# Kernel optimization log

Measured on AMD Instinct MI355X. Metric: run time of the kernel, lower is better.

## Reference

```python
import jax, jax.numpy as jnp
import numpy as np

EPS = 1e-5

def _layernorm(x, g, b):
    mu = jnp.mean(x, axis=-1, keepdims=True)
    var = jnp.mean((x - mu) ** 2, axis=-1, keepdims=True)
    return (x - mu) * jax.lax.rsqrt(var + EPS) * g + b

def setup_inputs() -> dict:
    key = jax.random.key(0)
    ks = jax.random.split(key, 12)
    B, N, C, n = 2, 1024, 256, 100
    x = jax.random.normal(ks[0], (B, N, C), dtype=jnp.float32)
    query = jax.random.normal(ks[1], (n, B, C), dtype=jnp.float32)
    policy = jax.random.uniform(ks[2], (B, N, 1), dtype=jnp.float32)
    s = lambda k, shp: jax.random.normal(k, shp, dtype=jnp.float32) * (1.0 / np.sqrt(shp[0]))
    return {
        "x": x, "query": query, "policy": policy,
        "ln_g": jnp.ones((C,), jnp.float32), "ln_b": jnp.zeros((C,), jnp.float32),
        "W_in": s(ks[3], (C, C)), "b_in": jnp.zeros((C,), jnp.float32),
        "W1": s(ks[4], (2 * C, C)), "b1": jnp.zeros((C,), jnp.float32),
        "W2": s(ks[5], (C, C // 2)), "b2": jnp.zeros((C // 2,), jnp.float32),
        "W3": s(ks[6], (C // 2, 2)), "b3": jnp.zeros((2,), jnp.float32),
    }

def reference(x, query, policy, ln_g, ln_b, W_in, b_in, W1, b1, W2, b2, W3, b3):
    B, N, C = x.shape
    n = query.shape[0]
    q = jnp.transpose(query, (1, 0, 2))  # [B, n, C]
    # in_conv: LayerNorm -> Linear -> GELU. The torch code repeats x across the
    # query dim first, but the math is identical per query, so compute once.
    h = jax.nn.gelu(_layernorm(x, ln_g, ln_b) @ W_in + b_in, approximate=False)  # [B, N, C]
    half = C // 2
    local_x = h[:, :, :half]  # [B, N, C/2]
    # policy-weighted masked pooling (policy identical across queries)
    glob = jnp.sum(h[:, :, half:] * policy, axis=1, keepdims=True) / jnp.sum(policy, axis=1, keepdims=True)  # [B, 1, C/2]
    feature = jnp.concatenate([
        jnp.broadcast_to(local_x[:, None, :, :], (B, n, N, half)),
        jnp.broadcast_to(glob[:, None, :, :], (B, n, N, half)),
        jnp.broadcast_to(q[:, :, None, :], (B, n, N, C)),
    ], axis=-1)  # [B, n, N, 2C]
    z = jax.nn.gelu(feature @ W1 + b1, approximate=False)
    z = jax.nn.gelu(z @ W2 + b2, approximate=False)
    z = z @ W3 + b3
    return jax.nn.log_softmax(z, axis=-1)  # [B, n, N, 2]
```

## Files before the change

### kernel.cpp

```cpp
#include <hip/hip_runtime.h>
#include <math.h>

#define BB 2
#define NN 1024
#define CC 256
#define NQ 100
#define HALF 128

typedef __attribute__((ext_vector_type(8))) short bf16x8;
typedef __attribute__((ext_vector_type(4))) float f32x4;

__device__ __forceinline__ float exp2_fast(float v) {
#if __has_builtin(__builtin_amdgcn_exp2f)
    return __builtin_amdgcn_exp2f(v);
#else
    return __expf(0.69314718056f * v);
#endif
}

__device__ __forceinline__ float gelu_fast(float x) {
    float x2 = x * x;
    float v = x * fmaf(0.10293942f, x2, 2.30211418f);
    float e = exp2_fast(v);
    float r = __builtin_amdgcn_rcpf(1.0f + e);
    return fmaf(-x, r, x);
}

__device__ __forceinline__ short f2bf(float f) {
    union { float f; unsigned u; } v; v.f = f;
    return (short)((v.u + 0x7FFFu + ((v.u >> 16) & 1u)) >> 16);
}

__global__ __launch_bounds__(256) void kA_fused(
        const float* __restrict__ x, const float* __restrict__ ln_g,
        const float* __restrict__ ln_b, const float* __restrict__ W_in,
        const float* __restrict__ b_in, const float* __restrict__ policy,
        const float* __restrict__ W1, float* __restrict__ At,
        float* __restrict__ gpart, float* __restrict__ ppart) {
    __shared__ float xst[CC][4];
    __shared__ float hst[HALF][4];
    int t = threadIdx.x;
    int wave = t >> 6, lane = t & 63;
    int blk = blockIdx.x;
    int row0 = blk * 4;
    const float* xr = x + (size_t)(row0 + wave) * CC;
    float v0 = xr[lane], v1 = xr[lane + 64], v2 = xr[lane + 128], v3 = xr[lane + 192];
    float s = v0 + v1 + v2 + v3;
    for (int off = 32; off; off >>= 1) s += __shfl_down(s, off);
    s = __shfl(s, 0);
    float mu = s * (1.0f / CC);
    float d0 = v0 - mu, d1 = v1 - mu, d2 = v2 - mu, d3 = v3 - mu;
    float vs = d0 * d0 + d1 * d1 + d2 * d2 + d3 * d3;
    for (int off = 32; off; off >>= 1) vs += __shfl_down(vs, off);
    vs = __shfl(vs, 0);
    float rstd = rsqrtf(vs * (1.0f / CC) + 1e-5f);
    xst[lane][wave]       = d0 * rstd * ln_g[lane]       + ln_b[lane];
    xst[lane + 64][wave]  = d1 * rstd * ln_g[lane + 64]  + ln_b[lane + 64];
    xst[lane + 128][wave] = d2 * rstd * ln_g[lane + 128] + ln_b[lane + 128];
    xst[lane + 192][wave] = d3 * rstd * ln_g[lane + 192] + ln_b[lane + 192];
    __syncthreads();
    float a0 = b_in[t], a1 = a0, a2 = a0, a3 = a0;
    #pragma unroll 8
    for (int k = 0; k < CC; ++k) {
        float4 xv = *(const float4*)xst[k];
        float wv = W_in[k * CC + t];
        a0 = fmaf(xv.x, wv, a0); a1 = fmaf(xv.y, wv, a1);
        a2 = fmaf(xv.z, wv, a2); a3 = fmaf(xv.w, wv, a3);
    }
    float h0 = gelu_fast(a0), h1 = gelu_fast(a1), h2 = gelu_fast(a2), h3 = gelu_fast(a3);
    float p0 = policy[row0], p1 = policy[row0 + 1], p2 = policy[row0 + 2], p3 = policy[row0 + 3];
    if (t < HALF) {
        hst[t][0] = h0; hst[t][1] = h1; hst[t][2] = h2; hst[t][3] = h3;
    } else {
        gpart[(size_t)blk * HALF + (t - HALF)] = h0 * p0 + h1 * p1 + h2 * p2 + h3 * p3;
    }
    if (t == 0) ppart[blk] = p0 + p1 + p2 + p3;
    __syncthreads();
    float c0 = 0, c1 = 0, c2 = 0, c3 = 0;
    #pragma unroll 8
    for (int k = 0; k < HALF; ++k) {
        float4 hv = *(const float4*)hst[k];
        float wv = W1[k * CC + t];
        c0 = fmaf(hv.x, wv, c0); c1 = fmaf(hv.y, wv, c1);
        c2 = fmaf(hv.z, wv, c2); c3 = fmaf(hv.w, wv, c3);
    }
    int b = row0 >> 10;
    int lr = row0 & (NN - 1);
    size_t tb = ((size_t)(b * 64 + (lr >> 4)) * 32 + (t >> 3)) * 128 + (t & 7);
    int r16 = lr & 15;
    At[tb + (r16 + 0) * 8] = c0;
    At[tb + (r16 + 1) * 8] = c1;
    At[tb + (r16 + 2) * 8] = c2;
    At[tb + (r16 + 3) * 8] = c3;
}

__global__ __launch_bounds__(256) void kB_qc_prep(
        const float* __restrict__ query, const float* __restrict__ W1,
        const float* __restrict__ W2, const float* __restrict__ gpart,
        const float* __restrict__ ppart, const float* __restrict__ b1,
        float* __restrict__ Qc, short* __restrict__ W2T) {
    int blk = blockIdx.x, t = threadIdx.x;
    if (blk >= BB * NQ) {
        int u = (blk - BB * NQ) * 256 + t;
        int n = u & 127;
        int kq = u >> 7;
        short4 v;
        v.x = f2bf(W2[(kq * 4 + 0) * HALF + n]);
        v.y = f2bf(W2[(kq * 4 + 1) * HALF + n]);
        v.z = f2bf(W2[(kq * 4 + 2) * HALF + n]);
        v.w = f2bf(W2[(kq * 4 + 3) * HALF + n]);
        *(short4*)(W2T + (size_t)((n >> 4) * 32 + (kq >> 1)) * 128
                   + (n & 15) * 8 + (kq & 1) * 4) = v;
        return;
    }
    __shared__ float gl2[2][HALF];
    __shared__ float gls[HALF];
    __shared__ float qs[CC];
    __shared__ float pss;
    int b = blk / NQ, i = blk % NQ;
    int c = t & 127, hh = t >> 7;
    {
        const float* gp = gpart + ((size_t)b * 256 + hh * 128) * HALF + c;
        float s = 0.f;
        #pragma unroll 16
        for (int ch = 0; ch < 128; ++ch) s += gp[(size_t)ch * HALF];
        gl2[hh][c] = s;
    }
    if (t < 64) {
        const float* pp = ppart + b * 256;
        float ps = pp[t] + pp[t + 64] + pp[t + 128] + pp[t + 192];
        for (int off = 32; off; off >>= 1) ps += __shfl_down(ps, off);
        if (t == 0) pss = ps;
    }
    qs[t] = query[(size_t)(i * BB + b) * CC + t];
    __syncthreads();
    if (t < HALF) gls[t] = (gl2[0][t] + gl2[1][t]) / pss;
    __syncthreads();
    float g = b1[t];
    #pragma unroll 8
    for (int k = 0; k < HALF; ++k)
        g = fmaf(gls[k], W1[(HALF + k) * CC + t], g);
    #pragma unroll 8
    for (int k = 0; k < CC; ++k)
        g = fmaf(qs[k], W1[(2 * HALF + k) * CC + t], g);
    Qc[(size_t)blk * CC + t] = g;
}

__global__ __launch_bounds__(256, 4) void k5_main(
        const float* __restrict__ At, const float* __restrict__ Qc,
        const short* __restrict__ W2T, const float* __restrict__ b2,
        const float* __restrict__ W3, const float* __restrict__ b3,
        float* __restrict__ out) {
    __shared__ short w2s[2][4096];

    int t = threadIdx.x;
    int lane = t & 63, w = t >> 6;
    int col16 = lane & 15, quad = lane >> 4;
    int blk = blockIdx.x;
    int jt = blk & 15;
    int iq = (blk >> 4) % NQ;
    int b  = blk / (16 * NQ);
    const float* Abase = At + ((size_t)(b * 64 + jt * 4 + w) * 32) * 128 + col16 * 8;
    const float* Qrow = Qc + (size_t)(b * NQ + iq) * CC;
    const short* Wg = W2T + (size_t)((t >> 6) * 32 + ((t >> 4) & 3)) * 128 + (t & 15) * 8;

    f32x4 acc[8];
    #pragma unroll
    for (int ni = 0; ni < 8; ++ni) acc[ni] = (f32x4){0.f, 0.f, 0.f, 0.f};

    bf16x8 nx0 = *(const bf16x8*)(Wg);
    bf16x8 nx1 = *(const bf16x8*)(Wg + 16384);
    float4 a0 = *(const float4*)(Abase + quad * 128);
    float4 a1 = *(const float4*)(Abase + quad * 128 + 4);
    float4 q0 = *(const float4*)(Qrow + quad * 8);
    float4 q1 = *(const float4*)(Qrow + quad * 8 + 4);
    *(bf16x8*)&w2s[0][t * 8] = nx0;
    *(bf16x8*)&w2s[0][2048 + t * 8] = nx1;
    nx0 = *(const bf16x8*)(Wg + 512);
    nx1 = *(const bf16x8*)(Wg + 16384 + 512);
    __syncthreads();

    #pragma unroll
    for (int kt = 0; kt < 8; ++kt) {
        int buf = kt & 1;
        if (kt < 7) {
            *(bf16x8*)&w2s[1 - buf][t * 8] = nx0;
            *(bf16x8*)&w2s[1 - buf][2048 + t * 8] = nx1;
        }
        if (kt < 6) {
            nx0 = *(const bf16x8*)(Wg + (kt + 2) * 512);
            nx1 = *(const bf16x8*)(Wg + 16384 + (kt + 2) * 512);
        }
        union { bf16x8 v; short s[8]; } fr;
        fr.s[0] = f2bf(gelu_fast(a0.x + q0.x));
        fr.s[1] = f2bf(gelu_fast(a0.y + q0.y));
        fr.s[2] = f2bf(gelu_fast(a0.z + q0.z));
        fr.s[3] = f2bf(gelu_fast(a0.w + q0.w));
        fr.s[4] = f2bf(gelu_fast(a1.x + q1.x));
        fr.s[5] = f2bf(gelu_fast(a1.y + q1.y));
        fr.s[6] = f2bf(gelu_fast(a1.z + q1.z));
        fr.s[7] = f2bf(gelu_fast(a1.w + q1.w));
        if (kt < 7) {
            const float* Ap = Abase + (size_t)((kt + 1) * 4 + quad) * 128;
            a0 = *(const float4*)(Ap);
            a1 = *(const float4*)(Ap + 4);
            q0 = *(const float4*)(Qrow + (kt + 1) * 32 + quad * 8);
            q1 = *(const float4*)(Qrow + (kt + 1) * 32 + quad * 8 + 4);
        }
        #pragma unroll
        for (int ni = 0; ni < 8; ++ni) {
            bf16x8 bv = *(const bf16x8*)&w2s[buf][(ni * 64 + lane) * 8];
            acc[ni] = __builtin_amdgcn_mfma_f32_16x16x32_bf16(fr.v, bv, acc[ni], 0, 0, 0);
        }
        if (kt < 7) __syncthreads();
    }

    float p0[4] = {0, 0, 0, 0}, p1[4] = {0, 0, 0, 0};
    #pragma unroll
    for (int ni = 0; ni < 8; ++ni) {
        int c = ni * 16 + col16;
        float bb = b2[c];
        float2 w3v = *(const float2*)(W3 + c * 2);
        #pragma unroll
        for (int r = 0; r < 4; ++r) {
            float z = gelu_fast(acc[ni][r] + bb);
            p0[r] = fmaf(z, w3v.x, p0[r]);
            p1[r] = fmaf(z, w3v.y, p1[r]);
        }
    }
    float b30 = b3[0], b31 = b3[1];
    #pragma unroll
    for (int r = 0; r < 4; ++r) {
        float s0 = p0[r], s1 = p1[r];
        #pragma unroll
        for (int off = 1; off < 16; off <<= 1) {
            s0 += __shfl_xor(s0, off);
            s1 += __shfl_xor(s1, off);
        }
        if (col16 == 0) {
            float z0 = s0 + b30, z1v = s1 + b31;
            float m = fmaxf(z0, z1v);
            float lse = m + __logf(__expf(z0 - m) + __expf(z1v - m));
            int j = jt * 64 + w * 16 + quad * 4 + r;
            *(float2*)(out + ((size_t)(b * NQ + iq) * NN + j) * 2) =
                make_float2(z0 - lse, z1v - lse);
        }
    }
}

extern "C" void kernel_launch(void* const* d_in, const int* in_sizes, int n_in,
                              void* d_out, int out_size, void* d_ws, size_t ws_size,
                              hipStream_t stream) {
    const float* x      = (const float*)d_in[0];
    const float* query  = (const float*)d_in[1];
    const float* policy = (const float*)d_in[2];
    const float* ln_g   = (const float*)d_in[3];
    const float* ln_b   = (const float*)d_in[4];
    const float* W_in   = (const float*)d_in[5];
    const float* b_in   = (const float*)d_in[6];
    const float* W1     = (const float*)d_in[7];
    const float* b1     = (const float*)d_in[8];
    const float* W2     = (const float*)d_in[9];
    const float* b2     = (const float*)d_in[10];
    const float* W3     = (const float*)d_in[11];
    const float* b3     = (const float*)d_in[12];
    float* out = (float*)d_out;

    float* ws    = (float*)d_ws;
    float* At    = ws;
    float* Qc    = ws + 524288;
    float* gpart = ws + 575488;
    float* ppart = ws + 641024;
    short* W2T   = (short*)(ws + 641536);

    kA_fused<<<512, 256, 0, stream>>>(x, ln_g, ln_b, W_in, b_in, policy,
                                      W1, At, gpart, ppart);
    kB_qc_prep<<<BB * NQ + 32, 256, 0, stream>>>(query, W1, W2, gpart, ppart,
                                                 b1, Qc, W2T);
    k5_main<<<BB * NQ * (NN / 64), 256, 0, stream>>>(At, Qc, W2T, b2, W3, b3, out);
}
```

Before: 155.4 us.

## Merge three kernels into one cooperative persistent kernel with grid syncs

Replaces the three separate launches (fused LN/in-conv, Qc prep, main MFMA kernel) with a single cooperative persistent kernel that loops over the former block indices and separates the stages with grid-wide syncs. The aim is to remove per-launch overhead and the gaps between launches. In exchange it adds grid-sync cost, an occupancy query on every call, and a grid capped at 1024 blocks, so the main stage's 3200 tiles run as strided loops rather than one block per tile. The first two stages get less parallelism than before, and grid sizing assumes 256 CUs.

```diff
diff --git a/kernel.cpp b/kernel.cpp
--- a/kernel.cpp
+++ b/kernel.cpp
@@ -1,5 +1,8 @@
 #include <hip/hip_runtime.h>
+#include <hip/hip_cooperative_groups.h>
 #include <math.h>
+
+namespace cg = cooperative_groups;
 
 #define BB 2
 #define NN 1024
@@ -31,219 +34,236 @@
     return (short)((v.u + 0x7FFFu + ((v.u >> 16) & 1u)) >> 16);
 }
 
-__global__ __launch_bounds__(256) void kA_fused(
+__global__ __launch_bounds__(256, 4) void mega(
         const float* __restrict__ x, const float* __restrict__ ln_g,
         const float* __restrict__ ln_b, const float* __restrict__ W_in,
         const float* __restrict__ b_in, const float* __restrict__ policy,
-        const float* __restrict__ W1, float* __restrict__ At,
-        float* __restrict__ gpart, float* __restrict__ ppart) {
-    __shared__ float xst[CC][4];
-    __shared__ float hst[HALF][4];
+        const float* __restrict__ query, const float* __restrict__ W1,
+        const float* __restrict__ W2, const float* __restrict__ b1,
+        const float* __restrict__ b2, const float* __restrict__ W3,
+        const float* __restrict__ b3, float* __restrict__ At,
+        float* __restrict__ Qc, float* __restrict__ gpart,
+        float* __restrict__ ppart, short* __restrict__ W2T,
+        float* __restrict__ out) {
+    cg::grid_group gg = cg::this_grid();
+    __shared__ __align__(16) char smem[16384];
     int t = threadIdx.x;
-    int wave = t >> 6, lane = t & 63;
-    int blk = blockIdx.x;
-    int row0 = blk * 4;
-    const float* xr = x + (size_t)(row0 + wave) * CC;
-    float v0 = xr[lane], v1 = xr[lane + 64], v2 = xr[lane + 128], v3 = xr[lane + 192];
-    float s = v0 + v1 + v2 + v3;
-    for (int off = 32; off; off >>= 1) s += __shfl_down(s, off);
-    s = __shfl(s, 0);
-    float mu = s * (1.0f / CC);
-    float d0 = v0 - mu, d1 = v1 - mu, d2 = v2 - mu, d3 = v3 - mu;
-    float vs = d0 * d0 + d1 * d1 + d2 * d2 + d3 * d3;
-    for (int off = 32; off; off >>= 1) vs += __shfl_down(vs, off);
-    vs = __shfl(vs, 0);
-    float rstd = rsqrtf(vs * (1.0f / CC) + 1e-5f);
-    xst[lane][wave]       = d0 * rstd * ln_g[lane]       + ln_b[lane];
-    xst[lane + 64][wave]  = d1 * rstd * ln_g[lane + 64]  + ln_b[lane + 64];
-    xst[lane + 128][wave] = d2 * rstd * ln_g[lane + 128] + ln_b[lane + 128];
-    xst[lane + 192][wave] = d3 * rstd * ln_g[lane + 192] + ln_b[lane + 192];
-    __syncthreads();
-    float a0 = b_in[t], a1 = a0, a2 = a0, a3 = a0;
-    #pragma unroll 8
-    for (int k = 0; k < CC; ++k) {
-        float4 xv = *(const float4*)xst[k];
-        float wv = W_in[k * CC + t];
-        a0 = fmaf(xv.x, wv, a0); a1 = fmaf(xv.y, wv, a1);
-        a2 = fmaf(xv.z, wv, a2); a3 = fmaf(xv.w, wv, a3);
-    }
-    float h0 = gelu_fast(a0), h1 = gelu_fast(a1), h2 = gelu_fast(a2), h3 = gelu_fast(a3);
-    float p0 = policy[row0], p1 = policy[row0 + 1], p2 = policy[row0 + 2], p3 = policy[row0 + 3];
-    if (t < HALF) {
-        hst[t][0] = h0; hst[t][1] = h1; hst[t][2] = h2; hst[t][3] = h3;
-    } else {
-        gpart[(size_t)blk * HALF + (t - HALF)] = h0 * p0 + h1 * p1 + h2 * p2 + h3 * p3;
-    }
-    if (t == 0) ppart[blk] = p0 + p1 + p2 + p3;
-    __syncthreads();
-    float c0 = 0, c1 = 0, c2 = 0, c3 = 0;
-    #pragma unroll 8
-    for (int k = 0; k < HALF; ++k) {
-        float4 hv = *(const float4*)hst[k];
-        float wv = W1[k * CC + t];
-        c0 = fmaf(hv.x, wv, c0); c1 = fmaf(hv.y, wv, c1);
-        c2 = fmaf(hv.z, wv, c2); c3 = fmaf(hv.w, wv, c3);
-    }
-    int b = row0 >> 10;
-    int lr = row0 & (NN - 1);
-    size_t tb = ((size_t)(b * 64 + (lr >> 4)) * 32 + (t >> 3)) * 128 + (t & 7);
-    int r16 = lr & 15;
-    At[tb + (r16 + 0) * 8] = c0;
-    At[tb + (r16 + 1) * 8] = c1;
-    At[tb + (r16 + 2) * 8] = c2;
-    At[tb + (r16 + 3) * 8] = c3;
-}
-
-__global__ __launch_bounds__(256) void kB_qc_prep(
-        const float* __restrict__ query, const float* __restrict__ W1,
-        const float* __restrict__ W2, const float* __restrict__ gpart,
-        const float* __restrict__ ppart, const float* __restrict__ b1,
-        float* __restrict__ Qc, short* __restrict__ W2T) {
-    int blk = blockIdx.x, t = threadIdx.x;
-    if (blk >= BB * NQ) {
-        int u = (blk - BB * NQ) * 256 + t;
-        int n = u & 127;
-        int kq = u >> 7;
-        short4 v;
-        v.x = f2bf(W2[(kq * 4 + 0) * HALF + n]);
-        v.y = f2bf(W2[(kq * 4 + 1) * HALF + n]);
-        v.z = f2bf(W2[(kq * 4 + 2) * HALF + n]);
-        v.w = f2bf(W2[(kq * 4 + 3) * HALF + n]);
-        *(short4*)(W2T + (size_t)((n >> 4) * 32 + (kq >> 1)) * 128
-                   + (n & 15) * 8 + (kq & 1) * 4) = v;
-        return;
-    }
-    __shared__ float gl2[2][HALF];
-    __shared__ float gls[HALF];
-    __shared__ float qs[CC];
-    __shared__ float pss;
-    int b = blk / NQ, i = blk % NQ;
-    int c = t & 127, hh = t >> 7;
+    int nb = gridDim.x;
+
     {
-        const float* gp = gpart + ((size_t)b * 256 + hh * 128) * HALF + c;
-        float s = 0.f;
-        #pragma unroll 16
-        for (int ch = 0; ch < 128; ++ch) s += gp[(size_t)ch * HALF];
-        gl2[hh][c] = s;
-    }
-    if (t < 64) {
-        const float* pp = ppart + b * 256;
-        float ps = pp[t] + pp[t + 64] + pp[t + 128] + pp[t + 192];
-        for (int off = 32; off; off >>= 1) ps += __shfl_down(ps, off);
-        if (t == 0) pss = ps;
-    }
-    qs[t] = query[(size_t)(i * BB + b) * CC + t];
-    __syncthreads();
-    if (t < HALF) gls[t] = (gl2[0][t] + gl2[1][t]) / pss;
-    __syncthreads();
-    float g = b1[t];
-    #pragma unroll 8
-    for (int k = 0; k < HALF; ++k)
-        g = fmaf(gls[k], W1[(HALF + k) * CC + t], g);
-    #pragma unroll 8
-    for (int k = 0; k < CC; ++k)
-        g = fmaf(qs[k], W1[(2 * HALF + k) * CC + t], g);
-    Qc[(size_t)blk * CC + t] = g;
-}
-
-__global__ __launch_bounds__(256, 4) void k5_main(
-        const float* __restrict__ At, const float* __restrict__ Qc,
-        const short* __restrict__ W2T, const float* __restrict__ b2,
-        const float* __restrict__ W3, const float* __restrict__ b3,
-        float* __restrict__ out) {
-    __shared__ short w2s[2][4096];
-
-    int t = threadIdx.x;
-    int lane = t & 63, w = t >> 6;
-    int col16 = lane & 15, quad = lane >> 4;
-    int blk = blockIdx.x;
-    int jt = blk & 15;
-    int iq = (blk >> 4) % NQ;
-    int b  = blk / (16 * NQ);
-    const float* Abase = At + ((size_t)(b * 64 + jt * 4 + w) * 32) * 128 + col16 * 8;
-    const float* Qrow = Qc + (size_t)(b * NQ + iq) * CC;
-    const short* Wg = W2T + (size_t)((t >> 6) * 32 + ((t >> 4) & 3)) * 128 + (t & 15) * 8;
-
-    f32x4 acc[8];
-    #pragma unroll
-    for (int ni = 0; ni < 8; ++ni) acc[ni] = (f32x4){0.f, 0.f, 0.f, 0.f};
-
-    bf16x8 nx0 = *(const bf16x8*)(Wg);
-    bf16x8 nx1 = *(const bf16x8*)(Wg + 16384);
-    float4 a0 = *(const float4*)(Abase + quad * 128);
-    float4 a1 = *(const float4*)(Abase + quad * 128 + 4);
-    float4 q0 = *(const float4*)(Qrow + quad * 8);
-    float4 q1 = *(const float4*)(Qrow + quad * 8 + 4);
-    *(bf16x8*)&w2s[0][t * 8] = nx0;
-    *(bf16x8*)&w2s[0][2048 + t * 8] = nx1;
-    nx0 = *(const bf16x8*)(Wg + 512);
-    nx1 = *(const bf16x8*)(Wg + 16384 + 512);
-    __syncthreads();
-
-    #pragma unroll
-    for (int kt = 0; kt < 8; ++kt) {
-        int buf = kt & 1;
-        if (kt < 7) {
-            *(bf16x8*)&w2s[1 - buf][t * 8] = nx0;
-            *(bf16x8*)&w2s[1 - buf][2048 + t * 8] = nx1;
-        }
-        if (kt < 6) {
-            nx0 = *(const bf16x8*)(Wg + (kt + 2) * 512);
-            nx1 = *(const bf16x8*)(Wg + 16384 + (kt + 2) * 512);
-        }
-        union { bf16x8 v; short s[8]; } fr;
-        fr.s[0] = f2bf(gelu_fast(a0.x + q0.x));
-        fr.s[1] = f2bf(gelu_fast(a0.y + q0.y));
-        fr.s[2] = f2bf(gelu_fast(a0.z + q0.z));
-        fr.s[3] = f2bf(gelu_fast(a0.w + q0.w));
-        fr.s[4] = f2bf(gelu_fast(a1.x + q1.x));
-        fr.s[5] = f2bf(gelu_fast(a1.y + q1.y));
-        fr.s[6] = f2bf(gelu_fast(a1.z + q1.z));
-        fr.s[7] = f2bf(gelu_fast(a1.w + q1.w));
-        if (kt < 7) {
-            const float* Ap = Abase + (size_t)((kt + 1) * 4 + quad) * 128;
-            a0 = *(const float4*)(Ap);
-            a1 = *(const float4*)(Ap + 4);
-            q0 = *(const float4*)(Qrow + (kt + 1) * 32 + quad * 8);
-            q1 = *(const float4*)(Qrow + (kt + 1) * 32 + quad * 8 + 4);
-        }
-        #pragma unroll
-        for (int ni = 0; ni < 8; ++ni) {
-            bf16x8 bv = *(const bf16x8*)&w2s[buf][(ni * 64 + lane) * 8];
-            acc[ni] = __builtin_amdgcn_mfma_f32_16x16x32_bf16(fr.v, bv, acc[ni], 0, 0, 0);
-        }
-        if (kt < 7) __syncthreads();
-    }
-
-    float p0[4] = {0, 0, 0, 0}, p1[4] = {0, 0, 0, 0};
-    #pragma unroll
-    for (int ni = 0; ni < 8; ++ni) {
-        int c = ni * 16 + col16;
-        float bb = b2[c];
-        float2 w3v = *(const float2*)(W3 + c * 2);
-        #pragma unroll
-        for (int r = 0; r < 4; ++r) {
-            float z = gelu_fast(acc[ni][r] + bb);
-            p0[r] = fmaf(z, w3v.x, p0[r]);
-            p1[r] = fmaf(z, w3v.y, p1[r]);
+        float* xst = (float*)smem;
+        float* hst = (float*)(smem + 4096);
+        for (int blk = blockIdx.x; blk < 544; blk += nb) {
+            if (blk >= 512) {
+                int u = (blk - 512) * 256 + t;
+                int n = u & 127;
+                int kq = u >> 7;
+                short4 v;
+                v.x = f2bf(W2[(kq * 4 + 0) * HALF + n]);
+                v.y = f2bf(W2[(kq * 4 + 1) * HALF + n]);
+                v.z = f2bf(W2[(kq * 4 + 2) * HALF + n]);
+                v.w = f2bf(W2[(kq * 4 + 3) * HALF + n]);
+                *(short4*)(W2T + (size_t)((n >> 4) * 32 + (kq >> 1)) * 128
+                           + (n & 15) * 8 + (kq & 1) * 4) = v;
+            } else {
+                int wave = t >> 6, lane = t & 63;
+                int row0 = blk * 4;
+                const float* xr = x + (size_t)(row0 + wave) * CC;
+                float v0 = xr[lane], v1 = xr[lane + 64];
+                float v2 = xr[lane + 128], v3 = xr[lane + 192];
+                float s = v0 + v1 + v2 + v3;
+                for (int off = 32; off; off >>= 1) s += __shfl_down(s, off);
+                s = __shfl(s, 0);
+                float mu = s * (1.0f / CC);
+                float d0 = v0 - mu, d1 = v1 - mu, d2 = v2 - mu, d3 = v3 - mu;
+                float vs = d0 * d0 + d1 * d1 + d2 * d2 + d3 * d3;
+                for (int off = 32; off; off >>= 1) vs += __shfl_down(vs, off);
+                vs = __shfl(vs, 0);
+                float rstd = rsqrtf(vs * (1.0f / CC) + 1e-5f);
+                xst[(lane)*4 + wave]       = d0 * rstd * ln_g[lane]       + ln_b[lane];
+                xst[(lane + 64)*4 + wave]  = d1 * rstd * ln_g[lane + 64]  + ln_b[lane + 64];
+                xst[(lane + 128)*4 + wave] = d2 * rstd * ln_g[lane + 128] + ln_b[lane + 128];
+                xst[(lane + 192)*4 + wave] = d3 * rstd * ln_g[lane + 192] + ln_b[lane + 192];
+                __syncthreads();
+                float a0 = b_in[t], a1 = a0, a2 = a0, a3 = a0;
+                #pragma unroll 8
+                for (int k = 0; k < CC; ++k) {
+                    float4 xv = *(const float4*)&xst[k * 4];
+                    float wv = W_in[k * CC + t];
+                    a0 = fmaf(xv.x, wv, a0); a1 = fmaf(xv.y, wv, a1);
+                    a2 = fmaf(xv.z, wv, a2); a3 = fmaf(xv.w, wv, a3);
+                }
+                float h0 = gelu_fast(a0), h1 = gelu_fast(a1);
+                float h2 = gelu_fast(a2), h3 = gelu_fast(a3);
+                float p0 = policy[row0], p1 = policy[row0 + 1];
+                float p2 = policy[row0 + 2], p3 = policy[row0 + 3];
+                if (t < HALF) {
+                    hst[t * 4 + 0] = h0; hst[t * 4 + 1] = h1;
+                    hst[t * 4 + 2] = h2; hst[t * 4 + 3] = h3;
+                } else {
+                    gpart[(size_t)blk * HALF + (t - HALF)] =
+                        h0 * p0 + h1 * p1 + h2 * p2 + h3 * p3;
+                }
+                if (t == 0) ppart[blk] = p0 + p1 + p2 + p3;
+                __syncthreads();
+                float c0 = 0, c1 = 0, c2 = 0, c3 = 0;
+                #pragma unroll 8
+                for (int k = 0; k < HALF; ++k) {
+                    float4 hv = *(const float4*)&hst[k * 4];
+                    float wv = W1[k * CC + t];
+                    c0 = fmaf(hv.x, wv, c0); c1 = fmaf(hv.y, wv, c1);
+                    c2 = fmaf(hv.z, wv, c2); c3 = fmaf(hv.w, wv, c3);
+                }
+                int b = row0 >> 10;
+                int lr = row0 & (NN - 1);
+                size_t tb = ((size_t)(b * 64 + (lr >> 4)) * 32 + (t >> 3)) * 128 + (t & 7);
+                int r16 = lr & 15;
+                At[tb + (r16 + 0) * 8] = c0;
+                At[tb + (r16 + 1) * 8] = c1;
+                At[tb + (r16 + 2) * 8] = c2;
+                At[tb + (r16 + 3) * 8] = c3;
+            }
+            __syncthreads();
         }
     }
-    float b30 = b3[0], b31 = b3[1];
-    #pragma unroll
-    for (int r = 0; r < 4; ++r) {
-        float s0 = p0[r], s1 = p1[r];
-        #pragma unroll
-        for (int off = 1; off < 16; off <<= 1) {
-            s0 += __shfl_xor(s0, off);
-            s1 += __shfl_xor(s1, off);
+    gg.sync();
+
+    {
+        float* gl2 = (float*)smem;
+        float* gls = (float*)(smem + 1024);
+        float* qs  = (float*)(smem + 1536);
+        float* pss = (float*)(smem + 2560);
+        for (int blk = blockIdx.x; blk < BB * NQ; blk += nb) {
+            int b = blk / NQ, i = blk % NQ;
+            int c = t & 127, hh = t >> 7;
+            {
+                const float* gp = gpart + ((size_t)b * 256 + hh * 128) * HALF + c;
+                float s = 0.f;
+                #pragma unroll 16
+                for (int ch = 0; ch < 128; ++ch) s += gp[(size_t)ch * HALF];
+                gl2[hh * HALF + c] = s;
+            }
+            if (t < 64) {
+                const float* pp = ppart + b * 256;
+                float ps = pp[t] + pp[t + 64] + pp[t + 128] + pp[t + 192];
+                for (int off = 32; off; off >>= 1) ps += __shfl_down(ps, off);
+                if (t == 0) pss[0] = ps;
+            }
+            qs[t] = query[(size_t)(i * BB + b) * CC + t];
+            __syncthreads();
+            if (t < HALF) gls[t] = (gl2[t] + gl2[HALF + t]) / pss[0];
+            __syncthreads();
+            float g = b1[t];
+            #pragma unroll 8
+            for (int k = 0; k < HALF; ++k)
+                g = fmaf(gls[k], W1[(HALF + k) * CC + t], g);
+            #pragma unroll 8
+            for (int k = 0; k < CC; ++k)
+                g = fmaf(qs[k], W1[(2 * HALF + k) * CC + t], g);
+            Qc[(size_t)blk * CC + t] = g;
+            __syncthreads();
         }
-        if (col16 == 0) {
-            float z0 = s0 + b30, z1v = s1 + b31;
-            float m = fmaxf(z0, z1v);
-            float lse = m + __logf(__expf(z0 - m) + __expf(z1v - m));
-            int j = jt * 64 + w * 16 + quad * 4 + r;
-            *(float2*)(out + ((size_t)(b * NQ + iq) * NN + j) * 2) =
-                make_float2(z0 - lse, z1v - lse);
+    }
+    gg.sync();
+
+    {
+        short* w2s = (short*)smem;
+        int lane = t & 63, w = t >> 6;
+        int col16 = lane & 15, quad = lane >> 4;
+        const short* Wg = W2T + (size_t)((t >> 6) * 32 + ((t >> 4) & 3)) * 128
+                          + (t & 15) * 8;
+        float b30 = b3[0], b31 = b3[1];
+        for (int blk = blockIdx.x; blk < BB * NQ * (NN / 64); blk += nb) {
+            int jt = blk & 15;
+            int iq = (blk >> 4) % NQ;
+            int b  = blk / (16 * NQ);
+            const float* Abase = At + ((size_t)(b * 64 + jt * 4 + w) * 32) * 128
+                                 + col16 * 8;
+            const float* Qrow = Qc + (size_t)(b * NQ + iq) * CC;
+
+            f32x4 acc[8];
+            #pragma unroll
+            for (int ni = 0; ni < 8; ++ni) acc[ni] = (f32x4){0.f, 0.f, 0.f, 0.f};
+
+            bf16x8 nx0 = *(const bf16x8*)(Wg);
+            bf16x8 nx1 = *(const bf16x8*)(Wg + 16384);
+            float4 a0 = *(const float4*)(Abase + quad * 128);
+            float4 a1 = *(const float4*)(Abase + quad * 128 + 4);
+            float4 q0 = *(const float4*)(Qrow + quad * 8);
+            float4 q1 = *(const float4*)(Qrow + quad * 8 + 4);
+            *(bf16x8*)&w2s[t * 8] = nx0;
+            *(bf16x8*)&w2s[2048 + t * 8] = nx1;
+            nx0 = *(const bf16x8*)(Wg + 512);
+            nx1 = *(const bf16x8*)(Wg + 16384 + 512);
+            __syncthreads();
+
+            #pragma unroll
+            for (int kt = 0; kt < 8; ++kt) {
+                int buf = kt & 1;
+                if (kt < 7) {
+                    *(bf16x8*)&w2s[(1 - buf) * 4096 + t * 8] = nx0;
+                    *(bf16x8*)&w2s[(1 - buf) * 4096 + 2048 + t * 8] = nx1;
+                }
+                if (kt < 6) {
+                    nx0 = *(const bf16x8*)(Wg + (kt + 2) * 512);
+                    nx1 = *(const bf16x8*)(Wg + 16384 + (kt + 2) * 512);
+                }
+                union { bf16x8 v; short s[8]; } fr;
+                fr.s[0] = f2bf(gelu_fast(a0.x + q0.x));
+                fr.s[1] = f2bf(gelu_fast(a0.y + q0.y));
+                fr.s[2] = f2bf(gelu_fast(a0.z + q0.z));
+                fr.s[3] = f2bf(gelu_fast(a0.w + q0.w));
+                fr.s[4] = f2bf(gelu_fast(a1.x + q1.x));
+                fr.s[5] = f2bf(gelu_fast(a1.y + q1.y));
+                fr.s[6] = f2bf(gelu_fast(a1.z + q1.z));
+                fr.s[7] = f2bf(gelu_fast(a1.w + q1.w));
+                if (kt < 7) {
+                    const float* Ap = Abase + (size_t)((kt + 1) * 4 + quad) * 128;
+                    a0 = *(const float4*)(Ap);
+                    a1 = *(const float4*)(Ap + 4);
+                    q0 = *(const float4*)(Qrow + (kt + 1) * 32 + quad * 8);
+                    q1 = *(const float4*)(Qrow + (kt + 1) * 32 + quad * 8 + 4);
+                }
+                #pragma unroll
+                for (int ni = 0; ni < 8; ++ni) {
+                    bf16x8 bv = *(const bf16x8*)&w2s[buf * 4096 + (ni * 64 + lane) * 8];
+                    acc[ni] = __builtin_amdgcn_mfma_f32_16x16x32_bf16(fr.v, bv,
+                                                                      acc[ni], 0, 0, 0);
+                }
+                if (kt < 7) __syncthreads();
+            }
+
+            float p0[4] = {0, 0, 0, 0}, p1[4] = {0, 0, 0, 0};
+            #pragma unroll
+            for (int ni = 0; ni < 8; ++ni) {
+                int c = ni * 16 + col16;
+                float bb = b2[c];
+                float2 w3v = *(const float2*)(W3 + c * 2);
+                #pragma unroll
+                for (int r = 0; r < 4; ++r) {
+                    float z = gelu_fast(acc[ni][r] + bb);
+                    p0[r] = fmaf(z, w3v.x, p0[r]);
+                    p1[r] = fmaf(z, w3v.y, p1[r]);
+                }
+            }
+            #pragma unroll
+            for (int r = 0; r < 4; ++r) {
+                float s0 = p0[r], s1 = p1[r];
+                #pragma unroll
+                for (int off = 1; off < 16; off <<= 1) {
+                    s0 += __shfl_xor(s0, off);
+                    s1 += __shfl_xor(s1, off);
+                }
+                if (col16 == 0) {
+                    float z0 = s0 + b30, z1v = s1 + b31;
+                    float m = fmaxf(z0, z1v);
+                    float lse = m + __logf(__expf(z0 - m) + __expf(z1v - m));
+                    int j = jt * 64 + w * 16 + quad * 4 + r;
+                    *(float2*)(out + ((size_t)(b * NQ + iq) * NN + j) * 2) =
+                        make_float2(z0 - lse, z1v - lse);
+                }
+            }
+            __syncthreads();
         }
     }
 }
@@ -273,9 +293,17 @@
     float* ppart = ws + 641024;
     short* W2T   = (short*)(ws + 641536);
 
-    kA_fused<<<512, 256, 0, stream>>>(x, ln_g, ln_b, W_in, b_in, policy,
-                                      W1, At, gpart, ppart);
-    kB_qc_prep<<<BB * NQ + 32, 256, 0, stream>>>(query, W1, W2, gpart, ppart,
-                                                 b1, Qc, W2T);
-    k5_main<<<BB * NQ * (NN / 64), 256, 0, stream>>>(At, Qc, W2T, b2, W3, b3, out);
-}
+    int nbpc = 0;
+    hipOccupancyMaxActiveBlocksPerMultiprocessor(&nbpc, mega, 256, 0);
+    if (nbpc < 1) nbpc = 1;
+    int grid = nbpc * 256;
+    if (grid > 1024) grid = 1024;
+
+    void* args[] = {
+        (void*)&x, (void*)&ln_g, (void*)&ln_b, (void*)&W_in, (void*)&b_in,
+        (void*)&policy, (void*)&query, (void*)&W1, (void*)&W2, (void*)&b1,
+        (void*)&b2, (void*)&W3, (void*)&b3, (void*)&At, (void*)&Qc,
+        (void*)&gpart, (void*)&ppart, (void*)&W2T, (void*)&out
+    };
+    hipLaunchCooperativeKernel((void*)mega, dim3(grid), dim3(256), args, 0, stream);
+}
```

Result: slower. 310.4 us (+99.7%).

## Process two M tiles per wave in main kernel and split launch by parity

Applied to the files above, without the earlier changes.

Each block of the main MFMA kernel now covers 128 rows instead of 64, with each wave computing two 16-row tiles that reuse the same W2 fragment read from LDS. This halves W2 LDS reads and staging per output and increases MFMA work per barrier. The grid is split into two launches selected by a parity argument, and bf16 packing uses paired conversion intrinsics. The doubled accumulators raise register pressure, and the extra launch adds overhead.

```diff
diff --git a/kernel.cpp b/kernel.cpp
--- a/kernel.cpp
+++ b/kernel.cpp
@@ -1,4 +1,5 @@
 #include <hip/hip_runtime.h>
+#include <hip/hip_bf16.h>
 #include <math.h>
 
 #define BB 2
@@ -67,12 +68,15 @@
         a0 = fmaf(xv.x, wv, a0); a1 = fmaf(xv.y, wv, a1);
         a2 = fmaf(xv.z, wv, a2); a3 = fmaf(xv.w, wv, a3);
     }
-    float h0 = gelu_fast(a0), h1 = gelu_fast(a1), h2 = gelu_fast(a2), h3 = gelu_fast(a3);
-    float p0 = policy[row0], p1 = policy[row0 + 1], p2 = policy[row0 + 2], p3 = policy[row0 + 3];
+    float h0 = gelu_fast(a0), h1 = gelu_fast(a1);
+    float h2 = gelu_fast(a2), h3 = gelu_fast(a3);
+    float p0 = policy[row0], p1 = policy[row0 + 1];
+    float p2 = policy[row0 + 2], p3 = policy[row0 + 3];
     if (t < HALF) {
         hst[t][0] = h0; hst[t][1] = h1; hst[t][2] = h2; hst[t][3] = h3;
     } else {
-        gpart[(size_t)blk * HALF + (t - HALF)] = h0 * p0 + h1 * p1 + h2 * p2 + h3 * p3;
+        gpart[(size_t)blk * HALF + (t - HALF)] =
+            h0 * p0 + h1 * p1 + h2 * p2 + h3 * p3;
     }
     if (t == 0) ppart[blk] = p0 + p1 + p2 + p3;
     __syncthreads();
@@ -150,28 +154,34 @@
         const float* __restrict__ At, const float* __restrict__ Qc,
         const short* __restrict__ W2T, const float* __restrict__ b2,
         const float* __restrict__ W3, const float* __restrict__ b3,
-        float* __restrict__ out) {
+        float* __restrict__ out, int parity) {
     __shared__ short w2s[2][4096];
 
     int t = threadIdx.x;
     int lane = t & 63, w = t >> 6;
     int col16 = lane & 15, quad = lane >> 4;
-    int blk = blockIdx.x;
-    int jt = blk & 15;
-    int iq = (blk >> 4) % NQ;
-    int b  = blk / (16 * NQ);
-    const float* Abase = At + ((size_t)(b * 64 + jt * 4 + w) * 32) * 128 + col16 * 8;
+    int blk = blockIdx.x * 2 + parity;
+    int jt = blk & 7;
+    int iq = (blk >> 3) % NQ;
+    int b  = blk / (8 * NQ);
+    const float* A0 = At + (size_t)(b * 64 + jt * 8 + w * 2) * 4096 + col16 * 8;
     const float* Qrow = Qc + (size_t)(b * NQ + iq) * CC;
-    const short* Wg = W2T + (size_t)((t >> 6) * 32 + ((t >> 4) & 3)) * 128 + (t & 15) * 8;
-
-    f32x4 acc[8];
+    const short* Wg = W2T + (size_t)((t >> 6) * 32 + ((t >> 4) & 3)) * 128
+                      + (t & 15) * 8;
+
+    f32x4 acc[2][8];
     #pragma unroll
-    for (int ni = 0; ni < 8; ++ni) acc[ni] = (f32x4){0.f, 0.f, 0.f, 0.f};
+    for (int mi = 0; mi < 2; ++mi)
+        #pragma unroll
+        for (int ni = 0; ni < 8; ++ni)
+            acc[mi][ni] = (f32x4){0.f, 0.f, 0.f, 0.f};
 
     bf16x8 nx0 = *(const bf16x8*)(Wg);
     bf16x8 nx1 = *(const bf16x8*)(Wg + 16384);
-    float4 a0 = *(const float4*)(Abase + quad * 128);
-    float4 a1 = *(const float4*)(Abase + quad * 128 + 4);
+    float4 a00 = *(const float4*)(A0 + quad * 128);
+    float4 a01 = *(const float4*)(A0 + quad * 128 + 4);
+    float4 a10 = *(const float4*)(A0 + 4096 + quad * 128);
+    float4 a11 = *(const float4*)(A0 + 4096 + quad * 128 + 4);
     float4 q0 = *(const float4*)(Qrow + quad * 8);
     float4 q1 = *(const float4*)(Qrow + quad * 8 + 4);
     *(bf16x8*)&w2s[0][t * 8] = nx0;
@@ -191,59 +201,75 @@
             nx0 = *(const bf16x8*)(Wg + (kt + 2) * 512);
             nx1 = *(const bf16x8*)(Wg + 16384 + (kt + 2) * 512);
         }
-        union { bf16x8 v; short s[8]; } fr;
-        fr.s[0] = f2bf(gelu_fast(a0.x + q0.x));
-        fr.s[1] = f2bf(gelu_fast(a0.y + q0.y));
-        fr.s[2] = f2bf(gelu_fast(a0.z + q0.z));
-        fr.s[3] = f2bf(gelu_fast(a0.w + q0.w));
-        fr.s[4] = f2bf(gelu_fast(a1.x + q1.x));
-        fr.s[5] = f2bf(gelu_fast(a1.y + q1.y));
-        fr.s[6] = f2bf(gelu_fast(a1.z + q1.z));
-        fr.s[7] = f2bf(gelu_fast(a1.w + q1.w));
+        union { bf16x8 v; __hip_bfloat162 h[4]; } f0, f1;
+        f0.h[0] = __float22bfloat162_rn(make_float2(gelu_fast(a00.x + q0.x),
+                                                   gelu_fast(a00.y + q0.y)));
+        f0.h[1] = __float22bfloat162_rn(make_float2(gelu_fast(a00.z + q0.z),
+                                                   gelu_fast(a00.w + q0.w)));
+        f0.h[2] = __float22bfloat162_rn(make_float2(gelu_fast(a01.x + q1.x),
+                                                   gelu_fast(a01.y + q1.y)));
+        f0.h[3] = __float22bfloat162_rn(make_float2(gelu_fast(a01.z + q1.z),
+                                                   gelu_fast(a01.w + q1.w)));
+        f1.h[0] = __float22bfloat162_rn(make_float2(gelu_fast(a10.x + q0.x),
+                                                   gelu_fast(a10.y + q0.y)));
+        f1.h[1] = __float22bfloat162_rn(make_float2(gelu_fast(a10.z + q0.z),
+                                                   gelu_fast(a10.w + q0.w)));
+        f1.h[2] = __float22bfloat162_rn(make_float2(gelu_fast(a11.x + q1.x),
+                                                   gelu_fast(a11.y + q1.y)));
+        f1.h[3] = __float22bfloat162_rn(make_float2(gelu_fast(a11.z + q1.z),
+                                                   gelu_fast(a11.w + q1.w)));
         if (kt < 7) {
-            const float* Ap = Abase + (size_t)((kt + 1) * 4 + quad) * 128;
-            a0 = *(const float4*)(Ap);
-            a1 = *(const float4*)(Ap + 4);
+            const float* Ap = A0 + (size_t)((kt + 1) * 4 + quad) * 128;
+            a00 = *(const float4*)(Ap);
+            a01 = *(const float4*)(Ap + 4);
+            a10 = *(const float4*)(Ap + 4096);
+            a11 = *(const float4*)(Ap + 4096 + 4);
             q0 = *(const float4*)(Qrow + (kt + 1) * 32 + quad * 8);
             q1 = *(const float4*)(Qrow + (kt + 1) * 32 + quad * 8 + 4);
         }
         #pragma unroll
         for (int ni = 0; ni < 8; ++ni) {
             bf16x8 bv = *(const bf16x8*)&w2s[buf][(ni * 64 + lane) * 8];
-            acc[ni] = __builtin_amdgcn_mfma_f32_16x16x32_bf16(fr.v, bv, acc[ni], 0, 0, 0);
+            acc[0][ni] = __builtin_amdgcn_mfma_f32_16x16x32_bf16(f0.v, bv,
+                                                                 acc[0][ni], 0, 0, 0);
+            acc[1][ni] = __builtin_amdgcn_mfma_f32_16x16x32_bf16(f1.v, bv,
+                                                                 acc[1][ni], 0, 0, 0);
         }
         if (kt < 7) __syncthreads();
     }
 
-    float p0[4] = {0, 0, 0, 0}, p1[4] = {0, 0, 0, 0};
+    float b30 = b3[0], b31 = b3[1];
     #pragma unroll
-    for (int ni = 0; ni < 8; ++ni) {
-        int c = ni * 16 + col16;
-        float bb = b2[c];
-        float2 w3v = *(const float2*)(W3 + c * 2);
+    for (int mi = 0; mi < 2; ++mi) {
+        float p0[4] = {0, 0, 0, 0}, p1[4] = {0, 0, 0, 0};
+        #pragma unroll
+        for (int ni = 0; ni < 8; ++ni) {
+            int c = ni * 16 + col16;
+            float bb = b2[c];
+            float2 w3v = *(const float2*)(W3 + c * 2);
+            #pragma unroll
+            for (int r = 0; r < 4; ++r) {
+                float z = gelu_fast(acc[mi][ni][r] + bb);
+                p0[r] = fmaf(z, w3v.x, p0[r]);
+                p1[r] = fmaf(z, w3v.y, p1[r]);
+            }
+        }
         #pragma unroll
         for (int r = 0; r < 4; ++r) {
-            float z = gelu_fast(acc[ni][r] + bb);
-            p0[r] = fmaf(z, w3v.x, p0[r]);
-            p1[r] = fmaf(z, w3v.y, p1[r]);
-        }
-    }
-    float b30 = b3[0], b31 = b3[1];
-    #pragma unroll
-    for (int r = 0; r < 4; ++r) {
-        float s0 = p0[r], s1 = p1[r];
-        #pragma unroll
-        for (int off = 1; off < 16; off <<= 1) {
-            s0 += __shfl_xor(s0, off);
-            s1 += __shfl_xor(s1, off);
-        }
-        if (col16 == 0) {
-            float z0 = s0 + b30, z1v = s1 + b31;
-            float m = fmaxf(z0, z1v);
-            float lse = m + __logf(__expf(z0 - m) + __expf(z1v - m));
-            int j = jt * 64 + w * 16 + quad * 4 + r;
-            *(float2*)(out + ((size_t)(b * NQ + iq) * NN + j) * 2) =
-                make_float2(z0 - lse, z1v - lse);
+            float s0 = p0[r], s1 = p1[r];
+            #pragma unroll
+            for (int off = 1; off < 16; off <<= 1) {
+                s0 += __shfl_xor(s0, off);
+                s1 += __shfl_xor(s1, off);
+            }
+            if (col16 == 0) {
+                float z0 = s0 + b30, z1v = s1 + b31;
+                float m = fmaxf(z0, z1v);
+                float lse = m + __logf(__expf(z0 - m) + __expf(z1v - m));
+                int j = jt * 128 + w * 32 + mi * 16 + quad * 4 + r;
+                *(float2*)(out + ((size_t)(b * NQ + iq) * NN + j) * 2) =
+                    make_float2(z0 - lse, z1v - lse);
+            }
         }
     }
 }
@@ -277,5 +303,6 @@
                                       W1, At, gpart, ppart);
     kB_qc_prep<<<BB * NQ + 32, 256, 0, stream>>>(query, W1, W2, gpart, ppart,
                                                  b1, Qc, W2T);
-    k5_main<<<BB * NQ * (NN / 64), 256, 0, stream>>>(At, Qc, W2T, b2, W3, b3, out);
-}
+    k5_main<<<800, 256, 0, stream>>>(At, Qc, W2T, b2, W3, b3, out, 0);
+    k5_main<<<800, 256, 0, stream>>>(At, Qc, W2T, b2, W3, b3, out, 1);
+}
```

After: 167.4 us. +7.7%, slower.

## Move query projection and W2 conversion into first kernel to shorten prep stage

Applied to the files above, without the earlier changes.

The query-dependent part of the first-layer projection (query times the W1 query block) and the W2 bf16 transpose now run as extra blocks of the first kernel, independent of the LayerNorm/in_conv work. The second kernel only adds the pooled global term to the precomputed query projection, shrinking its serial critical path. The main kernel also switches to the packed bf16x2 conversion intrinsic for the GELU fragments. This adds a workspace buffer and more blocks in the first launch.

```diff
diff --git a/kernel.cpp b/kernel.cpp
--- a/kernel.cpp
+++ b/kernel.cpp
@@ -1,4 +1,5 @@
 #include <hip/hip_runtime.h>
+#include <hip/hip_bf16.h>
 #include <math.h>
 
 #define BB 2
@@ -35,13 +36,41 @@
         const float* __restrict__ x, const float* __restrict__ ln_g,
         const float* __restrict__ ln_b, const float* __restrict__ W_in,
         const float* __restrict__ b_in, const float* __restrict__ policy,
-        const float* __restrict__ W1, float* __restrict__ At,
-        float* __restrict__ gpart, float* __restrict__ ppart) {
+        const float* __restrict__ query, const float* __restrict__ W1,
+        const float* __restrict__ W2, float* __restrict__ At,
+        float* __restrict__ Qcq, float* __restrict__ gpart,
+        float* __restrict__ ppart, short* __restrict__ W2T) {
     __shared__ float xst[CC][4];
     __shared__ float hst[HALF][4];
     int t = threadIdx.x;
+    int blk = blockIdx.x;
+    if (blk >= 712) {
+        int u = (blk - 712) * 256 + t;
+        int n = u & 127;
+        int kq = u >> 7;
+        short4 v;
+        v.x = f2bf(W2[(kq * 4 + 0) * HALF + n]);
+        v.y = f2bf(W2[(kq * 4 + 1) * HALF + n]);
+        v.z = f2bf(W2[(kq * 4 + 2) * HALF + n]);
+        v.w = f2bf(W2[(kq * 4 + 3) * HALF + n]);
+        *(short4*)(W2T + (size_t)((n >> 4) * 32 + (kq >> 1)) * 128
+                   + (n & 15) * 8 + (kq & 1) * 4) = v;
+        return;
+    }
+    if (blk >= 512) {
+        float* qs = (float*)xst;
+        int row = blk - 512;
+        int b = row / NQ, i = row % NQ;
+        qs[t] = query[(size_t)(i * BB + b) * CC + t];
+        __syncthreads();
+        float g = 0.f;
+        #pragma unroll 8
+        for (int k = 0; k < CC; ++k)
+            g = fmaf(qs[k], W1[(2 * HALF + k) * CC + t], g);
+        Qcq[(size_t)row * CC + t] = g;
+        return;
+    }
     int wave = t >> 6, lane = t & 63;
-    int blk = blockIdx.x;
     int row0 = blk * 4;
     const float* xr = x + (size_t)(row0 + wave) * CC;
     float v0 = xr[lane], v1 = xr[lane + 64], v2 = xr[lane + 128], v3 = xr[lane + 192];
@@ -67,12 +96,15 @@
         a0 = fmaf(xv.x, wv, a0); a1 = fmaf(xv.y, wv, a1);
         a2 = fmaf(xv.z, wv, a2); a3 = fmaf(xv.w, wv, a3);
     }
-    float h0 = gelu_fast(a0), h1 = gelu_fast(a1), h2 = gelu_fast(a2), h3 = gelu_fast(a3);
-    float p0 = policy[row0], p1 = policy[row0 + 1], p2 = policy[row0 + 2], p3 = policy[row0 + 3];
+    float h0 = gelu_fast(a0), h1 = gelu_fast(a1);
+    float h2 = gelu_fast(a2), h3 = gelu_fast(a3);
+    float p0 = policy[row0], p1 = policy[row0 + 1];
+    float p2 = policy[row0 + 2], p3 = policy[row0 + 3];
     if (t < HALF) {
         hst[t][0] = h0; hst[t][1] = h1; hst[t][2] = h2; hst[t][3] = h3;
     } else {
-        gpart[(size_t)blk * HALF + (t - HALF)] = h0 * p0 + h1 * p1 + h2 * p2 + h3 * p3;
+        gpart[(size_t)blk * HALF + (t - HALF)] =
+            h0 * p0 + h1 * p1 + h2 * p2 + h3 * p3;
     }
     if (t == 0) ppart[blk] = p0 + p1 + p2 + p3;
     __syncthreads();
@@ -94,30 +126,15 @@
     At[tb + (r16 + 3) * 8] = c3;
 }
 
-__global__ __launch_bounds__(256) void kB_qc_prep(
-        const float* __restrict__ query, const float* __restrict__ W1,
-        const float* __restrict__ W2, const float* __restrict__ gpart,
+__global__ __launch_bounds__(256) void kB_combine(
+        const float* __restrict__ W1, const float* __restrict__ gpart,
         const float* __restrict__ ppart, const float* __restrict__ b1,
-        float* __restrict__ Qc, short* __restrict__ W2T) {
-    int blk = blockIdx.x, t = threadIdx.x;
-    if (blk >= BB * NQ) {
-        int u = (blk - BB * NQ) * 256 + t;
-        int n = u & 127;
-        int kq = u >> 7;
-        short4 v;
-        v.x = f2bf(W2[(kq * 4 + 0) * HALF + n]);
-        v.y = f2bf(W2[(kq * 4 + 1) * HALF + n]);
-        v.z = f2bf(W2[(kq * 4 + 2) * HALF + n]);
-        v.w = f2bf(W2[(kq * 4 + 3) * HALF + n]);
-        *(short4*)(W2T + (size_t)((n >> 4) * 32 + (kq >> 1)) * 128
-                   + (n & 15) * 8 + (kq & 1) * 4) = v;
-        return;
-    }
+        const float* __restrict__ Qcq, float* __restrict__ Qc) {
     __shared__ float gl2[2][HALF];
     __shared__ float gls[HALF];
-    __shared__ float qs[CC];
     __shared__ float pss;
-    int b = blk / NQ, i = blk % NQ;
+    int blk = blockIdx.x, t = threadIdx.x;
+    int b = blk / NQ;
     int c = t & 127, hh = t >> 7;
     {
         const float* gp = gpart + ((size_t)b * 256 + hh * 128) * HALF + c;
@@ -132,17 +149,13 @@
         for (int off = 32; off; off >>= 1) ps += __shfl_down(ps, off);
         if (t == 0) pss = ps;
     }
-    qs[t] = query[(size_t)(i * BB + b) * CC + t];
     __syncthreads();
     if (t < HALF) gls[t] = (gl2[0][t] + gl2[1][t]) / pss;
     __syncthreads();
-    float g = b1[t];
+    float g = b1[t] + Qcq[(size_t)blk * CC + t];
     #pragma unroll 8
     for (int k = 0; k < HALF; ++k)
         g = fmaf(gls[k], W1[(HALF + k) * CC + t], g);
-    #pragma unroll 8
-    for (int k = 0; k < CC; ++k)
-        g = fmaf(qs[k], W1[(2 * HALF + k) * CC + t], g);
     Qc[(size_t)blk * CC + t] = g;
 }
 
@@ -162,7 +175,8 @@
     int b  = blk / (16 * NQ);
     const float* Abase = At + ((size_t)(b * 64 + jt * 4 + w) * 32) * 128 + col16 * 8;
     const float* Qrow = Qc + (size_t)(b * NQ + iq) * CC;
-    const short* Wg = W2T + (size_t)((t >> 6) * 32 + ((t >> 4) & 3)) * 128 + (t & 15) * 8;
+    const short* Wg = W2T + (size_t)((t >> 6) * 32 + ((t >> 4) & 3)) * 128
+                      + (t & 15) * 8;
 
     f32x4 acc[8];
     #pragma unroll
@@ -191,15 +205,15 @@
             nx0 = *(const bf16x8*)(Wg + (kt + 2) * 512);
             nx1 = *(const bf16x8*)(Wg + 16384 + (kt + 2) * 512);
         }
-        union { bf16x8 v; short s[8]; } fr;
-        fr.s[0] = f2bf(gelu_fast(a0.x + q0.x));
-        fr.s[1] = f2bf(gelu_fast(a0.y + q0.y));
-        fr.s[2] = f2bf(gelu_fast(a0.z + q0.z));
-        fr.s[3] = f2bf(gelu_fast(a0.w + q0.w));
-        fr.s[4] = f2bf(gelu_fast(a1.x + q1.x));
-        fr.s[5] = f2bf(gelu_fast(a1.y + q1.y));
-        fr.s[6] = f2bf(gelu_fast(a1.z + q1.z));
-        fr.s[7] = f2bf(gelu_fast(a1.w + q1.w));
+        union { bf16x8 v; __hip_bfloat162 h[4]; } fr;
+        fr.h[0] = __float22bfloat162_rn(make_float2(gelu_fast(a0.x + q0.x),
+                                                   gelu_fast(a0.y + q0.y)));
+        fr.h[1] = __float22bfloat162_rn(make_float2(gelu_fast(a0.z + q0.z),
+                                                   gelu_fast(a0.w + q0.w)));
+        fr.h[2] = __float22bfloat162_rn(make_float2(gelu_fast(a1.x + q1.x),
+                                                   gelu_fast(a1.y + q1.y)));
+        fr.h[3] = __float22bfloat162_rn(make_float2(gelu_fast(a1.z + q1.z),
+                                                   gelu_fast(a1.w + q1.w)));
         if (kt < 7) {
             const float* Ap = Abase + (size_t)((kt + 1) * 4 + quad) * 128;
             a0 = *(const float4*)(Ap);
@@ -210,7 +224,8 @@
         #pragma unroll
         for (int ni = 0; ni < 8; ++ni) {
             bf16x8 bv = *(const bf16x8*)&w2s[buf][(ni * 64 + lane) * 8];
-            acc[ni] = __builtin_amdgcn_mfma_f32_16x16x32_bf16(fr.v, bv, acc[ni], 0, 0, 0);
+            acc[ni] = __builtin_amdgcn_mfma_f32_16x16x32_bf16(fr.v, bv,
+                                                              acc[ni], 0, 0, 0);
         }
         if (kt < 7) __syncthreads();
     }
@@ -268,14 +283,14 @@
 
     float* ws    = (float*)d_ws;
     float* At    = ws;
-    float* Qc    = ws + 524288;
-    float* gpart = ws + 575488;
-    float* ppart = ws + 641024;
-    short* W2T   = (short*)(ws + 641536);
-
-    kA_fused<<<512, 256, 0, stream>>>(x, ln_g, ln_b, W_in, b_in, policy,
-                                      W1, At, gpart, ppart);
-    kB_qc_prep<<<BB * NQ + 32, 256, 0, stream>>>(query, W1, W2, gpart, ppart,
-                                                 b1, Qc, W2T);
-    k5_main<<<BB * NQ * (NN / 64), 256, 0, stream>>>(At, Qc, W2T, b2, W3, b3, out);
-}
+    float* Qcq   = ws + 524288;
+    float* Qc    = ws + 575488;
+    float* gpart = ws + 626688;
+    float* ppart = ws + 692224;
+    short* W2T   = (short*)(ws + 692736);
+
+    kA_fused<<<744, 256, 0, stream>>>(x, ln_g, ln_b, W_in, b_in, policy,
+                                      query, W1, W2, At, Qcq, gpart, ppart, W2T);
+    kB_combine<<<BB * NQ, 256, 0, stream>>>(W1, gpart, ppart, b1, Qcq, Qc);
+    k5_main<<<3200, 256, 0, stream>>>(At, Qc, W2T, b2, W3, b3, out);
+}
```

Measured after the change: 142.2 us (median of 2 runs). -8.5%, faster.
